# Performance work log

Measured on AMD Instinct MI355X. Metric: run time of the kernel, lower is better.

## Reference

```python
import jax, jax.numpy as jnp
import numpy as np

EPS = 1e-8  # torch F.cosine_similarity default eps
MARGIN = 1.0


def _pair_indices(p_lens, n_lens):
    """Build gather indices for the ragged all-pairs (positive x negative) expansion.
    For batch i, pair order is lexicographic (j, k): positive j repeated n_i times,
    negative segment tiled p_i times -- exactly matching the torch repeat/repeat_interleave.
    Host-side numpy (lens are concrete integers)."""
    p = np.asarray(p_lens, dtype=np.int64)
    n = np.asarray(n_lens, dtype=np.int64)
    pairs = p * n                                   # per-example pair counts
    total = int(pairs.sum())
    p_off = np.concatenate([[0], np.cumsum(p)[:-1]])
    n_off = np.concatenate([[0], np.cumsum(n)[:-1]])
    pair_off = np.concatenate([[0], np.cumsum(pairs)[:-1]])
    a_idx = np.repeat(np.arange(len(p)), pairs)     # [total]
    t = np.arange(total) - np.repeat(pair_off, pairs)   # local pair position in [0, p_i*n_i)
    n_rep = np.repeat(n, pairs)
    j = t // n_rep                                  # positive index within segment
    k = t % n_rep                                   # negative index within segment
    p_idx = np.repeat(p_off, pairs) + j
    n_idx = np.repeat(n_off, pairs) + k
    return jnp.asarray(a_idx), jnp.asarray(p_idx), jnp.asarray(n_idx)


def _cosine(x, y):
    dot = jnp.sum(x * y, axis=-1)
    nx = jnp.linalg.norm(x, axis=-1)
    ny = jnp.linalg.norm(y, axis=-1)
    return dot / jnp.maximum(nx * ny, EPS)


def setup_inputs() -> dict:
    rng = np.random.default_rng(0)
    bs, dim = 1024, 768
    p_lens = rng.integers(1, 13, size=bs)
    n_lens = rng.integers(1, 13, size=bs)
    key = jax.random.key(0)
    k1, k2, k3 = jax.random.split(key, 3)
    anchor = jax.random.normal(k1, (bs, dim), dtype=jnp.float32)
    positive = jax.random.normal(k2, (int(p_lens.sum()), dim), dtype=jnp.float32)
    negative = jax.random.normal(k3, (int(n_lens.sum()), dim), dtype=jnp.float32)
    return {
        "anchor": anchor,
        "positive": positive,
        "negative": negative,
        "positive_lens": jnp.asarray(p_lens, dtype=jnp.int32),
        "negative_lens": jnp.asarray(n_lens, dtype=jnp.int32),
    }


def reference(anchor, positive, negative, positive_lens, negative_lens):
    a_idx, p_idx, n_idx = _pair_indices(positive_lens, negative_lens)
    a = anchor[a_idx]       # [total_pairs, dim]
    pp = positive[p_idx]
    nn_ = negative[n_idx]
    d_ap = 1.0 - _cosine(a, pp)
    d_an = 1.0 - _cosine(a, nn_)
    # TripletMarginWithDistanceLoss, swap=False, reduction='mean'
    loss = jnp.mean(jnp.maximum(d_ap - d_an + MARGIN, 0.0))
    return loss
```

## Files before the change

### kernel.cpp

```cpp
#include <hip/hip_runtime.h>
#include <hip/hip_bf16.h>

#define DIM 768
#define EPS 1e-8f

__global__ __launch_bounds__(512, 8) void triplet_partials(
    const float* __restrict__ anchor, const float* __restrict__ positive,
    const float* __restrict__ negative,
    const int* __restrict__ p_lens, const int* __restrict__ n_lens,
    float* __restrict__ partials, int bs)
{
    const int b = blockIdx.x;
    const int tid = threadIdx.x;
    const int wave = tid >> 6;
    const int lane = tid & 63;

    __shared__ float sA[DIM];
    __shared__ float sCos[32];
    __shared__ float sRedF[8];
    __shared__ int   sRedI[8][3];
    __shared__ float sAnorm;
    __shared__ int   sPO, sNO, sTot;

    const float4* a4 = (const float4*)(anchor + (size_t)b * DIM);
    float asq = 0.0f;
    for (int q = tid; q < DIM / 4; q += 512) {
        float4 v = a4[q];
        ((float4*)sA)[q] = v;
        asq += v.x * v.x + v.y * v.y + v.z * v.z + v.w * v.w;
    }

    int pre_p = 0, pre_n = 0, tot = 0;
    for (int i = tid; i < bs; i += 512) {
        int p = p_lens[i];
        int n = n_lens[i];
        if (i < b) { pre_p += p; pre_n += n; }
        tot += p * n;
    }

    #pragma unroll
    for (int s = 32; s > 0; s >>= 1) {
        asq   += __shfl_xor(asq, s);
        pre_p += __shfl_xor(pre_p, s);
        pre_n += __shfl_xor(pre_n, s);
        tot   += __shfl_xor(tot, s);
    }
    if (lane == 0) {
        sRedF[wave] = asq;
        sRedI[wave][0] = pre_p;
        sRedI[wave][1] = pre_n;
        sRedI[wave][2] = tot;
    }
    __syncthreads();
    if (tid == 0) {
        float a = 0.0f; int o0 = 0, o1 = 0, o2 = 0;
        #pragma unroll
        for (int w = 0; w < 8; ++w) {
            a  += sRedF[w];
            o0 += sRedI[w][0];
            o1 += sRedI[w][1];
            o2 += sRedI[w][2];
        }
        sAnorm = sqrtf(a);
        sPO = o0; sNO = o1; sTot = o2;
    }
    const int pl = p_lens[b];
    const int nl = n_lens[b];
    __syncthreads();
    const float an = sAnorm;
    const int po = sPO, no = sNO;

    const int nvec = pl + nl;
    for (int v = wave; v < nvec; v += 8) {
        const float* x = (v < pl)
            ? positive + (size_t)(po + v) * DIM
            : negative + (size_t)(no + (v - pl)) * DIM;
        const float4* x4 = (const float4*)x;
        float dot = 0.0f, nx = 0.0f;
        #pragma unroll
        for (int q = 0; q < 3; ++q) {
            float4 xv = x4[lane + 64 * q];
            float4 av = ((const float4*)sA)[lane + 64 * q];
            dot += av.x * xv.x + av.y * xv.y + av.z * xv.z + av.w * xv.w;
            nx  += xv.x * xv.x + xv.y * xv.y + xv.z * xv.z + xv.w * xv.w;
        }
        #pragma unroll
        for (int s = 32; s > 0; s >>= 1) {
            dot += __shfl_xor(dot, s);
            nx  += __shfl_xor(nx, s);
        }
        if (lane == 0) sCos[v] = dot / fmaxf(an * sqrtf(nx), EPS);
    }
    __syncthreads();

    const int pairs = pl * nl;
    float s = 0.0f;
    for (int t = tid; t < pairs; t += 512) {
        int j = t / nl;
        int k = t - j * nl;
        s += fmaxf(sCos[pl + k] - sCos[j] + 1.0f, 0.0f);
    }
    #pragma unroll
    for (int sh = 32; sh > 0; sh >>= 1) s += __shfl_xor(s, sh);
    if (lane == 0) sRedF[wave] = s;
    __syncthreads();
    if (tid == 0) {
        float blk = 0.0f;
        #pragma unroll
        for (int w = 0; w < 8; ++w) blk += sRedF[w];
        partials[b] = blk / (float)sTot;
    }
}

__global__ __launch_bounds__(1024) void reduce_partials(
    const float* __restrict__ partials, float* __restrict__ out, int bs)
{
    const int tid = threadIdx.x;
    const int wave = tid >> 6;
    const int lane = tid & 63;
    __shared__ float sw[16];

    float v = (tid < bs) ? partials[tid] : 0.0f;
    #pragma unroll
    for (int s = 32; s > 0; s >>= 1) v += __shfl_xor(v, s);
    if (lane == 0) sw[wave] = v;
    __syncthreads();
    if (tid == 0) {
        float t = 0.0f;
        #pragma unroll
        for (int i = 0; i < 16; ++i) t += sw[i];
        *out = t;
    }
}

extern "C" void kernel_launch(void* const* d_in, const int* in_sizes, int n_in,
                              void* d_out, int out_size, void* d_ws, size_t ws_size,
                              hipStream_t stream) {
    const float* anchor   = (const float*)d_in[0];
    const float* positive = (const float*)d_in[1];
    const float* negative = (const float*)d_in[2];
    const int*   p_lens   = (const int*)d_in[3];
    const int*   n_lens   = (const int*)d_in[4];
    float* out = (float*)d_out;

    const int bs = in_sizes[3];
    float* partials = (float*)d_ws;

    triplet_partials<<<bs, 512, 0, stream>>>(anchor, positive, negative,
                                             p_lens, n_lens, partials, bs);
    reduce_partials<<<1, 1024, 0, stream>>>(partials, out, bs);
}
```

Before: 90.64 us.

## Compute per-block prefix and anchor norm redundantly per wave, drop block barriers

Each wave now loads the anchor row into registers and computes the anchor norm, prefix offsets and total pair count on its own with int4 loads and wave shuffles. This removes the shared-memory anchor copy and the first two block-wide barriers. Each wave also processes two positive/negative vectors per iteration so more loads are in flight, and the final reduce kernel uses 256 threads with float4 loads. The cost is that every wave now reads the full length arrays, multiplying global (mostly cached) traffic by eight, and register pressure goes up.

```diff
diff --git a/kernel.cpp b/kernel.cpp
--- a/kernel.cpp
+++ b/kernel.cpp
@@ -15,28 +15,37 @@
     const int wave = tid >> 6;
     const int lane = tid & 63;
 
-    __shared__ float sA[DIM];
     __shared__ float sCos[32];
     __shared__ float sRedF[8];
-    __shared__ int   sRedI[8][3];
-    __shared__ float sAnorm;
-    __shared__ int   sPO, sNO, sTot;
 
     const float4* a4 = (const float4*)(anchor + (size_t)b * DIM);
-    float asq = 0.0f;
-    for (int q = tid; q < DIM / 4; q += 512) {
-        float4 v = a4[q];
-        ((float4*)sA)[q] = v;
-        asq += v.x * v.x + v.y * v.y + v.z * v.z + v.w * v.w;
-    }
+    const float4 av0 = a4[lane];
+    const float4 av1 = a4[lane + 64];
+    const float4 av2 = a4[lane + 128];
 
     int pre_p = 0, pre_n = 0, tot = 0;
-    for (int i = tid; i < bs; i += 512) {
-        int p = p_lens[i];
-        int n = n_lens[i];
+    const int4* p4 = (const int4*)p_lens;
+    const int4* n4 = (const int4*)n_lens;
+    const int nq = bs >> 2;
+    for (int q = lane; q < nq; q += 64) {
+        int4 pv = p4[q];
+        int4 nv = n4[q];
+        int base = q << 2;
+        pre_p += (base     < b ? pv.x : 0) + (base + 1 < b ? pv.y : 0)
+               + (base + 2 < b ? pv.z : 0) + (base + 3 < b ? pv.w : 0);
+        pre_n += (base     < b ? nv.x : 0) + (base + 1 < b ? nv.y : 0)
+               + (base + 2 < b ? nv.z : 0) + (base + 3 < b ? nv.w : 0);
+        tot += pv.x * nv.x + pv.y * nv.y + pv.z * nv.z + pv.w * nv.w;
+    }
+    for (int i = (nq << 2) + lane; i < bs; i += 64) {
+        int p = p_lens[i], n = n_lens[i];
         if (i < b) { pre_p += p; pre_n += n; }
         tot += p * n;
     }
+
+    float asq = av0.x*av0.x + av0.y*av0.y + av0.z*av0.z + av0.w*av0.w
+              + av1.x*av1.x + av1.y*av1.y + av1.z*av1.z + av1.w*av1.w
+              + av2.x*av2.x + av2.y*av2.y + av2.z*av2.z + av2.w*av2.w;
 
     #pragma unroll
     for (int s = 32; s > 0; s >>= 1) {
@@ -45,51 +54,58 @@
         pre_n += __shfl_xor(pre_n, s);
         tot   += __shfl_xor(tot, s);
     }
-    if (lane == 0) {
-        sRedF[wave] = asq;
-        sRedI[wave][0] = pre_p;
-        sRedI[wave][1] = pre_n;
-        sRedI[wave][2] = tot;
-    }
-    __syncthreads();
-    if (tid == 0) {
-        float a = 0.0f; int o0 = 0, o1 = 0, o2 = 0;
-        #pragma unroll
-        for (int w = 0; w < 8; ++w) {
-            a  += sRedF[w];
-            o0 += sRedI[w][0];
-            o1 += sRedI[w][1];
-            o2 += sRedI[w][2];
-        }
-        sAnorm = sqrtf(a);
-        sPO = o0; sNO = o1; sTot = o2;
-    }
+    const float an = sqrtf(asq);
+    const int po = pre_p, no = pre_n;
+
     const int pl = p_lens[b];
     const int nl = n_lens[b];
-    __syncthreads();
-    const float an = sAnorm;
-    const int po = sPO, no = sNO;
+    const int nvec = pl + nl;
 
-    const int nvec = pl + nl;
-    for (int v = wave; v < nvec; v += 8) {
-        const float* x = (v < pl)
-            ? positive + (size_t)(po + v) * DIM
-            : negative + (size_t)(no + (v - pl)) * DIM;
-        const float4* x4 = (const float4*)x;
-        float dot = 0.0f, nx = 0.0f;
-        #pragma unroll
-        for (int q = 0; q < 3; ++q) {
-            float4 xv = x4[lane + 64 * q];
-            float4 av = ((const float4*)sA)[lane + 64 * q];
-            dot += av.x * xv.x + av.y * xv.y + av.z * xv.z + av.w * xv.w;
-            nx  += xv.x * xv.x + xv.y * xv.y + xv.z * xv.z + xv.w * xv.w;
+    for (int v0 = wave * 2; v0 < nvec; v0 += 16) {
+        const int v1 = v0 + 1;
+        const bool has1 = (v1 < nvec);
+
+        const float* x0p = (v0 < pl)
+            ? positive + (size_t)(po + v0) * DIM
+            : negative + (size_t)(no + (v0 - pl)) * DIM;
+        const float4 x0a = ((const float4*)x0p)[lane];
+        const float4 x0b = ((const float4*)x0p)[lane + 64];
+        const float4 x0c = ((const float4*)x0p)[lane + 128];
+
+        float4 x1a = make_float4(0.f,0.f,0.f,0.f), x1b = x1a, x1c = x1a;
+        if (has1) {
+            const float* x1p = (v1 < pl)
+                ? positive + (size_t)(po + v1) * DIM
+                : negative + (size_t)(no + (v1 - pl)) * DIM;
+            x1a = ((const float4*)x1p)[lane];
+            x1b = ((const float4*)x1p)[lane + 64];
+            x1c = ((const float4*)x1p)[lane + 128];
         }
+
+        float d0 = av0.x*x0a.x + av0.y*x0a.y + av0.z*x0a.z + av0.w*x0a.w
+                 + av1.x*x0b.x + av1.y*x0b.y + av1.z*x0b.z + av1.w*x0b.w
+                 + av2.x*x0c.x + av2.y*x0c.y + av2.z*x0c.z + av2.w*x0c.w;
+        float q0 = x0a.x*x0a.x + x0a.y*x0a.y + x0a.z*x0a.z + x0a.w*x0a.w
+                 + x0b.x*x0b.x + x0b.y*x0b.y + x0b.z*x0b.z + x0b.w*x0b.w
+                 + x0c.x*x0c.x + x0c.y*x0c.y + x0c.z*x0c.z + x0c.w*x0c.w;
+        float d1 = av0.x*x1a.x + av0.y*x1a.y + av0.z*x1a.z + av0.w*x1a.w
+                 + av1.x*x1b.x + av1.y*x1b.y + av1.z*x1b.z + av1.w*x1b.w
+                 + av2.x*x1c.x + av2.y*x1c.y + av2.z*x1c.z + av2.w*x1c.w;
+        float q1 = x1a.x*x1a.x + x1a.y*x1a.y + x1a.z*x1a.z + x1a.w*x1a.w
+                 + x1b.x*x1b.x + x1b.y*x1b.y + x1b.z*x1b.z + x1b.w*x1b.w
+                 + x1c.x*x1c.x + x1c.y*x1c.y + x1c.z*x1c.z + x1c.w*x1c.w;
+
         #pragma unroll
         for (int s = 32; s > 0; s >>= 1) {
-            dot += __shfl_xor(dot, s);
-            nx  += __shfl_xor(nx, s);
+            d0 += __shfl_xor(d0, s);
+            q0 += __shfl_xor(q0, s);
+            d1 += __shfl_xor(d1, s);
+            q1 += __shfl_xor(q1, s);
         }
-        if (lane == 0) sCos[v] = dot / fmaxf(an * sqrtf(nx), EPS);
+        if (lane == 0) {
+            sCos[v0] = d0 / fmaxf(an * sqrtf(q0), EPS);
+            if (has1) sCos[v1] = d1 / fmaxf(an * sqrtf(q1), EPS);
+        }
     }
     __syncthreads();
 
@@ -108,29 +124,31 @@
         float blk = 0.0f;
         #pragma unroll
         for (int w = 0; w < 8; ++w) blk += sRedF[w];
-        partials[b] = blk / (float)sTot;
+        partials[b] = blk / (float)tot;
     }
 }
 
-__global__ __launch_bounds__(1024) void reduce_partials(
+__global__ __launch_bounds__(256) void reduce_partials(
     const float* __restrict__ partials, float* __restrict__ out, int bs)
 {
     const int tid = threadIdx.x;
     const int wave = tid >> 6;
     const int lane = tid & 63;
-    __shared__ float sw[16];
+    __shared__ float sw[4];
 
-    float v = (tid < bs) ? partials[tid] : 0.0f;
+    float s = 0.0f;
+    const float4* p4 = (const float4*)partials;
+    const int nq = bs >> 2;
+    for (int q = tid; q < nq; q += 256) {
+        float4 v = p4[q];
+        s += v.x + v.y + v.z + v.w;
+    }
+    for (int i = (nq << 2) + tid; i < bs; i += 256) s += partials[i];
     #pragma unroll
-    for (int s = 32; s > 0; s >>= 1) v += __shfl_xor(v, s);
-    if (lane == 0) sw[wave] = v;
+    for (int sh = 32; sh > 0; sh >>= 1) s += __shfl_xor(s, sh);
+    if (lane == 0) sw[wave] = s;
     __syncthreads();
-    if (tid == 0) {
-        float t = 0.0f;
-        #pragma unroll
-        for (int i = 0; i < 16; ++i) t += sw[i];
-        *out = t;
-    }
+    if (tid == 0) *out = sw[0] + sw[1] + sw[2] + sw[3];
 }
 
 extern "C" void kernel_launch(void* const* d_in, const int* in_sizes, int n_in,
@@ -148,5 +166,5 @@
 
     triplet_partials<<<bs, 512, 0, stream>>>(anchor, positive, negative,
                                              p_lens, n_lens, partials, bs);
-    reduce_partials<<<1, 1024, 0, stream>>>(partials, out, bs);
+    reduce_partials<<<1, 256, 0, stream>>>(partials, out, bs);
 }
```

Measured after the change: 92.05 us. Within noise of the previous version (+1.6%).
